# Performance work log

Measured on AMD Instinct MI355X. Metric: run time of the kernel, lower is better.

The kernel has to match this reference:

```python
import jax, jax.numpy as jnp
import numpy as np

B, T, V, E, H, L = 64, 512, 50000, 256, 256, 9


def _lstm_dir(x, w_ih, w_hh, b, reverse):
    # x: [B,T,I]; w_ih: [4H,I]; w_hh: [4H,H]; b: [4H]. PyTorch gate order i,f,g,o.
    Bm, Hm = x.shape[0], w_hh.shape[1]
    gx = jnp.einsum('bti,gi->btg', x, w_ih) + b  # [B,T,4H] precomputed input proj

    def step(carry, g_t):
        h, c = carry
        gates = g_t + h @ w_hh.T
        i, f, g, o = jnp.split(gates, 4, axis=-1)
        c = jax.nn.sigmoid(f) * c + jax.nn.sigmoid(i) * jnp.tanh(g)
        h = jax.nn.sigmoid(o) * jnp.tanh(c)
        return (h, c), h

    init = (jnp.zeros((Bm, Hm), x.dtype), jnp.zeros((Bm, Hm), x.dtype))
    _, hs = jax.lax.scan(step, init, jnp.swapaxes(gx, 0, 1), reverse=reverse)
    return jnp.swapaxes(hs, 0, 1)  # [B,T,H]


def _bilstm_layer(x, w_ih, w_hh, b):
    fwd = _lstm_dir(x, w_ih[0], w_hh[0], b[0], False)
    bwd = _lstm_dir(x, w_ih[1], w_hh[1], b[1], True)
    return jnp.concatenate([fwd, bwd], axis=-1)  # [B,T,2H]


def _crf_nll(emissions, labels, mask, trans, start_trans, end_trans):
    # emissions: [B,T,L]; labels: [B,T] int; mask: [B,T] (mask[:,0] assumed 1)
    maskf = mask.astype(emissions.dtype)
    # gold path score
    em_lab = jnp.take_along_axis(emissions, labels[..., None], axis=2)[..., 0]  # [B,T]
    trans_sc = trans[labels[:, :-1], labels[:, 1:]]  # [B,T-1]
    score = start_trans[labels[:, 0]] + em_lab[:, 0] \
        + jnp.sum((trans_sc + em_lab[:, 1:]) * maskf[:, 1:], axis=1)
    last_idx = jnp.sum(mask, axis=1).astype(jnp.int32) - 1
    last_lab = jnp.take_along_axis(labels, last_idx[:, None].astype(labels.dtype), axis=1)[:, 0]
    score = score + end_trans[last_lab]
    # log-partition via forward algorithm (scan over time)
    alpha0 = start_trans[None, :] + emissions[:, 0]  # [B,L]

    def step(alpha, xs):
        em_t, m_t = xs
        new = jax.nn.logsumexp(alpha[:, :, None] + trans[None], axis=1) + em_t
        alpha = jnp.where(m_t[:, None] > 0, new, alpha)
        return alpha, None

    alpha, _ = jax.lax.scan(
        step, alpha0,
        (jnp.swapaxes(emissions[:, 1:], 0, 1), jnp.swapaxes(mask[:, 1:], 0, 1)))
    logZ = jax.nn.logsumexp(alpha + end_trans[None, :], axis=1)  # [B]
    return -(score - logZ).mean()


def setup_inputs() -> dict:
    key = jax.random.key(0)
    ks = jax.random.split(key, 16)
    s = 0.05
    inp = {
        'input_ids': jax.random.randint(ks[0], (B, T), 0, V),
        'attention_mask': jnp.ones((B, T), jnp.int32),
        'labels': jax.random.randint(ks[1], (B, T), 0, L),
        'emb': jax.random.normal(ks[2], (V, E), jnp.float32) * s,
        # layer 0: input size E; layer 1: input size 2H. [dir, 4H, in]
        'w_ih0': jax.random.normal(ks[3], (2, 4 * H, E), jnp.float32) * s,
        'w_hh0': jax.random.normal(ks[4], (2, 4 * H, H), jnp.float32) * s,
        'b0': jax.random.normal(ks[5], (2, 4 * H), jnp.float32) * s,
        'w_ih1': jax.random.normal(ks[6], (2, 4 * H, 2 * H), jnp.float32) * s,
        'w_hh1': jax.random.normal(ks[7], (2, 4 * H, H), jnp.float32) * s,
        'b1': jax.random.normal(ks[8], (2, 4 * H), jnp.float32) * s,
        'lin_w': jax.random.normal(ks[9], (L, 2 * H), jnp.float32) * s,
        'lin_b': jax.random.normal(ks[10], (L,), jnp.float32) * s,
        'trans': jax.random.normal(ks[11], (L, L), jnp.float32) * 0.1,
        'start_trans': jax.random.normal(ks[12], (L,), jnp.float32) * 0.1,
        'end_trans': jax.random.normal(ks[13], (L,), jnp.float32) * 0.1,
    }
    return inp


def reference(input_ids, attention_mask, labels, emb, w_ih0, w_hh0, b0,
              w_ih1, w_hh1, b1, lin_w, lin_b, trans, start_trans, end_trans):
    x = emb[input_ids]                       # [B,T,E]
    x = _bilstm_layer(x, w_ih0, w_hh0, b0)   # [B,T,2H]
    x = _bilstm_layer(x, w_ih1, w_hh1, b1)   # [B,T,2H]
    emissions = x @ lin_w.T + lin_b          # [B,T,L]
    loss = _crf_nll(emissions, labels, attention_mask, trans, start_trans, end_trans)
    return loss
```

## Files before the change

### kernel.cpp

```cpp
#include <hip/hip_runtime.h>
#include <stdint.h>
#include <stddef.h>

#define B_ 64
#define T_ 512
#define E_ 256
#define H_ 256
#define L_ 9
#define BT (B_*T_)
#define G4 1024
#define N2 2048

typedef short    bf16x8  __attribute__((ext_vector_type(8)));
typedef float    f32x4   __attribute__((ext_vector_type(4)));
typedef int      i32x4   __attribute__((ext_vector_type(4)));
typedef int      i32x8   __attribute__((ext_vector_type(8)));
typedef unsigned short u16x8 __attribute__((ext_vector_type(8)));

__device__ __forceinline__ unsigned short f2bf(float x){
    unsigned u = __builtin_bit_cast(unsigned, x);
    u += 0x7fffu + ((u >> 16) & 1u);
    return (unsigned short)(u >> 16);
}
__device__ __forceinline__ float bf2f(unsigned short h){
    unsigned u = ((unsigned)h) << 16;
    return __builtin_bit_cast(float, u);
}

__device__ __forceinline__ unsigned char f32_e4m3(float x){
    unsigned b = __builtin_bit_cast(unsigned, x);
    unsigned s = b >> 31;
    float a = fabsf(x);
    if (a >= 448.f) return (unsigned char)((s<<7) | 0x7E);
    int E = (int)((b>>23)&255) - 127;
    if (E < -6) E = -6;
    int qi = (int)rintf(a * exp2f((float)(3 - E)));
    if (qi >= 16){ qi >>= 1; ++E; }
    if (qi == 0) return (unsigned char)(s<<7);
    unsigned mag = (qi >= 8) ? ((((unsigned)(E + 7)) << 3) | (unsigned)(qi - 8))
                             : (unsigned)qi;
    return (unsigned char)((s<<7) | mag);
}

__device__ __forceinline__ float sigm(float x){
    return __builtin_amdgcn_rcpf(1.f + __expf(-x));
}
__device__ __forceinline__ float tanh_(float x){
    float e = __expf(2.f*x);
    return 1.f - 2.f*__builtin_amdgcn_rcpf(e + 1.f);
}

__device__ __forceinline__ unsigned char f32_fp8(float x){
#if __has_builtin(__builtin_amdgcn_cvt_pk_fp8_f32)
    return (unsigned char)(__builtin_amdgcn_cvt_pk_fp8_f32(x, x, 0, false) & 0xff);
#else
    return f32_e4m3(x);
#endif
}

__device__ __forceinline__ void lds_load16(void* lds, const void* g){
    __builtin_amdgcn_global_load_lds(
        (const __attribute__((address_space(1))) void*)g,
        (__attribute__((address_space(3))) void*)lds, 16, 0, 0);
}

__device__ __forceinline__ void barrier_lds(){
    asm volatile("s_waitcnt lgkmcnt(0)" ::: "memory");
    __builtin_amdgcn_s_barrier();
    __builtin_amdgcn_sched_barrier(0);
}

__global__ void k_embed(const int* __restrict__ ids, const float* __restrict__ emb,
                        unsigned char* __restrict__ x0){
    int bt = blockIdx.x;
    int e  = threadIdx.x;
    int id = ids[bt];
    x0[(size_t)bt*E_ + e] = f32_e4m3(emb[(size_t)id*E_ + e]);
}

__global__ void k_pack_wih(const float* __restrict__ in, unsigned char* __restrict__ out, int K){
    int p = blockIdx.y;
    int k = blockIdx.x*256 + threadIdx.x;
    int dirc = p >> 10, pp = p & 1023;
    int wv = pp >> 7, rem = pp & 127;
    int ulx = rem >> 3, uh = (rem >> 2) & 1, g = rem & 3;
    int orig = dirc*1024 + g*256 + wv*32 + uh*16 + ulx;
    out[(size_t)p*K + k] = f32_e4m3(in[(size_t)orig*K + k]);
}

__global__ void k_pack_bias(const float* __restrict__ b, float* __restrict__ bp){
    int p = blockIdx.x*256 + threadIdx.x;
    int dirc = p >> 10, pp = p & 1023;
    int wv = pp >> 7, rem = pp & 127;
    int ulx = rem >> 3, uh = (rem >> 2) & 1, g = rem & 3;
    int orig = dirc*1024 + g*256 + wv*32 + uh*16 + ulx;
    bp[p] = b[orig];
}

__global__ void k_pack_wfp8(const float* __restrict__ whh, unsigned char* __restrict__ wpk){
    int idx = blockIdx.x*256 + threadIdx.x;
    int lane = idx & 63;
    int uh   = (idx >> 6) & 1;
    int g    = (idx >> 7) & 3;
    int kt   = (idx >> 9) & 1;
    int wv   = (idx >> 10) & 7;
    int dir  = (idx >> 13) & 1;
    int ulx = lane & 15, hi4 = lane >> 4;
    int row = g*256 + wv*32 + uh*16 + ulx;
    int k0 = kt*128 + hi4*32;
    const float* src = whh + ((size_t)dir*G4 + row)*H_ + k0;
    unsigned char* dst = wpk + (size_t)idx*32;
    #pragma unroll
    for (int q = 0; q < 32; ++q) dst[q] = f32_e4m3(src[q]);
}

__global__ __launch_bounds__(256) void k_gemm_fp8(const unsigned char* __restrict__ A,
                                                  const unsigned char* __restrict__ Bm,
                                                  const float* __restrict__ bias,
                                                  unsigned short* __restrict__ C,
                                                  int M, int N, int K){
    __shared__ __align__(16) unsigned char As[2][16384];
    __shared__ __align__(16) unsigned char Bs[2][16384];
    int tid = threadIdx.x, lane = tid & 63, w = tid >> 6;
    int wm = w >> 1, wn = w & 1;
    int nwg = gridDim.x, qch = nwg >> 3;
    int nid = (blockIdx.x & 7)*qch + (blockIdx.x >> 3);
    int tileM = (nid >> 4) * 128, tileN = (nid & 15) * 128;
    int nC = K >> 7;

    auto stage = [&](int c, int buf){
        #pragma unroll
        for (int p = 0; p < 4; ++p){
            int idx = (p*256 + tid)*16;
            int ks = idx >> 12, rem = idx & 4095, row = rem >> 5;
            int jsrc = (rem & 16) ^ ((row & 4) << 2);
            lds_load16(&As[buf][idx], A + (size_t)(tileM + row)*K + c*128 + ks*32 + jsrc);
            lds_load16(&Bs[buf][idx], Bm + (size_t)(tileN + row)*K + c*128 + ks*32 + jsrc);
        }
    };

    stage(0, 0);
    __syncthreads();
    f32x4 acc[4][4] = {};
    for (int c = 0; c < nC; ++c){
        int buf = c & 1;
        if (c + 1 < nC) stage(c + 1, buf ^ 1);
        int ks = lane >> 4, m15 = lane & 15;
        i32x8 af[4], bfv[4];
        #pragma unroll
        for (int mf = 0; mf < 4; ++mf){
            int r = wm*64 + mf*16 + m15;
            int base = ks*4096 + r*32, sw = (r & 4) << 2;
            i32x4 lo = *(const i32x4*)(&As[buf][base + sw]);
            i32x4 hi = *(const i32x4*)(&As[buf][base + (16 ^ sw)]);
            af[mf] = __builtin_shufflevector(lo, hi, 0,1,2,3,4,5,6,7);
        }
        #pragma unroll
        for (int nf = 0; nf < 4; ++nf){
            int r = wn*64 + nf*16 + m15;
            int base = ks*4096 + r*32, sw = (r & 4) << 2;
            i32x4 lo = *(const i32x4*)(&Bs[buf][base + sw]);
            i32x4 hi = *(const i32x4*)(&Bs[buf][base + (16 ^ sw)]);
            bfv[nf] = __builtin_shufflevector(lo, hi, 0,1,2,3,4,5,6,7);
        }
        #pragma unroll
        for (int mf = 0; mf < 4; ++mf)
            #pragma unroll
            for (int nf = 0; nf < 4; ++nf)
                acc[mf][nf] = __builtin_amdgcn_mfma_scale_f32_16x16x128_f8f6f4(
                                  af[mf], bfv[nf], acc[mf][nf],
                                  0, 0, 0, 0x7f7f7f7f, 0, 0x7f7f7f7f);
        __syncthreads();
    }
    #pragma unroll
    for (int mf = 0; mf < 4; ++mf){
        #pragma unroll
        for (int nf = 0; nf < 4; ++nf){
            int row0 = tileM + wm*64 + mf*16 + (lane >> 4)*4;
            int col  = tileN + wn*64 + nf*16 + (lane & 15);
            float bv = bias[col];
            #pragma unroll
            for (int r = 0; r < 4; ++r)
                C[(size_t)(row0 + r)*N + col] = f2bf(acc[mf][nf][r] + bv);
        }
    }
}

template<typename OutT>
__global__ __launch_bounds__(512, 2)
void k_rec_mfma(const unsigned short* __restrict__ gx,
                const unsigned char* __restrict__ wpk,
                OutT* __restrict__ out){
    int blk = blockIdx.x;
    int dir = blk & 1, bg = blk >> 1;
    int tid = threadIdx.x, lane = tid & 63, w = tid >> 6;
    int ul = lane & 15, hi4 = lane >> 4;
    int batch = bg*4 + hi4;

    __shared__ __align__(16) unsigned char hlds[2][32][16][8];
    {
        unsigned long long* hz = (unsigned long long*)hlds;
        for (int i = tid; i < 1024; i += 512) hz[i] = 0ull;
    }

    i32x8 wf[2][4][2];
    {
        const i32x8* wb = (const i32x8*)wpk;
        #pragma unroll
        for (int kt = 0; kt < 2; ++kt)
            #pragma unroll
            for (int g = 0; g < 4; ++g)
                #pragma unroll
                for (int uh = 0; uh < 2; ++uh)
                    wf[kt][g][uh] = wb[((((size_t)(dir*8 + w)*2 + kt)*4 + g)*2 + uh)*64 + lane];
    }
    __syncthreads();

    const unsigned short* gp = gx + (size_t)(batch*T_ + (dir ? T_-1 : 0))*N2
                                  + dir*1024 + w*128 + ul*8;
    ptrdiff_t dstep = dir ? -(ptrdiff_t)N2 : (ptrdiff_t)N2;

    u16x8 gxr = *(const u16x8*)gp;
    float c0 = 0.f, c1 = 0.f;
    int u0 = w*32 + ul, u1 = u0 + 16;
    OutT* ob = out + (size_t)batch*T_*512 + dir*256;

#define REC_STEP(SV, BUF)                                                          \
    {                                                                              \
        const unsigned long long* hrow = (const unsigned long long*)&hlds[BUF][0][0][0]; \
        unsigned long long a00 = hrow[(hi4*4 + 0)*16 + ul];                        \
        unsigned long long a01 = hrow[(hi4*4 + 1)*16 + ul];                        \
        unsigned long long a02 = hrow[(hi4*4 + 2)*16 + ul];                        \
        unsigned long long a03 = hrow[(hi4*4 + 3)*16 + ul];                        \
        unsigned long long a10 = hrow[(16 + hi4*4 + 0)*16 + ul];                   \
        unsigned long long a11 = hrow[(16 + hi4*4 + 1)*16 + ul];                   \
        unsigned long long a12 = hrow[(16 + hi4*4 + 2)*16 + ul];                   \
        unsigned long long a13 = hrow[(16 + hi4*4 + 3)*16 + ul];                   \
        i32x8 af0 = (i32x8){ (int)a00, (int)(a00>>32), (int)a01, (int)(a01>>32),   \
                             (int)a02, (int)(a02>>32), (int)a03, (int)(a03>>32) }; \
        i32x8 af1 = (i32x8){ (int)a10, (int)(a10>>32), (int)a11, (int)(a11>>32),   \
                             (int)a12, (int)(a12>>32), (int)a13, (int)(a13>>32) }; \
        gp += dstep;                                                               \
        u16x8 gxn = *(const u16x8*)gp;                                             \
        f32x4 acc0[4], acc1[4];                                                    \
        _Pragma("unroll")                                                          \
        for (int g = 0; g < 4; ++g){                                               \
            acc0[g] = (f32x4){ bf2f(gxr[g]),   0.f, 0.f, 0.f };                    \
            acc1[g] = (f32x4){ bf2f(gxr[4+g]), 0.f, 0.f, 0.f };                    \
        }                                                                          \
                                                          \
        __builtin_amdgcn_s_setprio(1);                                             \
        _Pragma("unroll")                                                          \
        for (int g = 0; g < 4; ++g)                                                \
            acc0[g] = __builtin_amdgcn_mfma_scale_f32_16x16x128_f8f6f4(            \
                          af0, wf[0][g][0], acc0[g], 0, 0, 0, 0x7f7f7f7f, 0, 0x7f7f7f7f); \
        _Pragma("unroll")                                                          \
        for (int g = 0; g < 4; ++g)                                                \
            acc0[g] = __builtin_amdgcn_mfma_scale_f32_16x16x128_f8f6f4(            \
                          af1, wf[1][g][0], acc0[g], 0, 0, 0, 0x7f7f7f7f, 0, 0x7f7f7f7f); \
        __builtin_amdgcn_s_setprio(0);                                             \
                                           \
        float h0;                                                                  \
        {                                                                          \
            float xi = acc0[0][0], xf = acc0[1][0], xg = acc0[2][0], xo = acc0[3][0]; \
            c0 = sigm(xf)*c0 + sigm(xi)*tanh_(xg);                                 \
            h0 = sigm(xo)*tanh_(c0);                                               \
        }                                                                          \
        unsigned char hb0 = f32_fp8(h0);                                           \
        hlds[BUF^1][u0>>3][hi4*4][u0&7] = hb0;                                     \
                                                          \
        __builtin_amdgcn_s_setprio(1);                                             \
        _Pragma("unroll")                                                          \
        for (int g = 0; g < 4; ++g)                                                \
            acc1[g] = __builtin_amdgcn_mfma_scale_f32_16x16x128_f8f6f4(            \
                          af0, wf[0][g][1], acc1[g], 0, 0, 0, 0x7f7f7f7f, 0, 0x7f7f7f7f); \
        _Pragma("unroll")                                                          \
        for (int g = 0; g < 4; ++g)                                                \
            acc1[g] = __builtin_amdgcn_mfma_scale_f32_16x16x128_f8f6f4(            \
                          af1, wf[1][g][1], acc1[g], 0, 0, 0, 0x7f7f7f7f, 0, 0x7f7f7f7f); \
        __builtin_amdgcn_s_setprio(0);                                             \
        float h1;                                                                  \
        {                                                                          \
            float xi = acc1[0][0], xf = acc1[1][0], xg = acc1[2][0], xo = acc1[3][0]; \
            c1 = sigm(xf)*c1 + sigm(xi)*tanh_(xg);                                 \
            h1 = sigm(xo)*tanh_(c1);                                               \
        }                                                                          \
        unsigned char hb1 = f32_fp8(h1);                                           \
        hlds[BUF^1][u1>>3][hi4*4][u1&7] = hb1;                                     \
        barrier_lds();                                                             \
                       \
        int tt = dir ? (T_-1-(SV)) : (SV);                                         \
        if constexpr (sizeof(OutT) == 1){                                          \
            ((unsigned char*)ob)[(size_t)tt*512 + u0] = hb0;                       \
            ((unsigned char*)ob)[(size_t)tt*512 + u1] = hb1;                       \
        } else {                                                                   \
            ob[(size_t)tt*512 + u0] = (OutT)f2bf(h0);                              \
            ob[(size_t)tt*512 + u1] = (OutT)f2bf(h1);                              \
        }                                                                          \
        gxr = gxn;                                                                 \
    }

    for (int s = 0; s < T_; s += 2){
        REC_STEP(s, 0)
        REC_STEP(s+1, 1)
    }
#undef REC_STEP
}

__global__ __launch_bounds__(256) void k_linear(const unsigned short* __restrict__ x,
                                                const float* __restrict__ w,
                                                const float* __restrict__ bias,
                                                float* __restrict__ em){
    int wv = threadIdx.x >> 6, lane = threadIdx.x & 63;
    int bt = blockIdx.x*4 + wv;
    u16x8 xv = *(const u16x8*)(x + (size_t)bt*(2*H_) + lane*8);
    float xf[8];
    #pragma unroll
    for (int j = 0; j < 8; ++j) xf[j] = bf2f(xv[j]);
    #pragma unroll
    for (int l = 0; l < L_; ++l){
        const float4* wp = (const float4*)(w + (size_t)l*(2*H_) + lane*8);
        float4 wa = wp[0], wb = wp[1];
        float p = xf[0]*wa.x + xf[1]*wa.y + xf[2]*wa.z + xf[3]*wa.w
                + xf[4]*wb.x + xf[5]*wb.y + xf[6]*wb.z + xf[7]*wb.w;
        #pragma unroll
        for (int o = 32; o; o >>= 1) p += __shfl_xor(p, o);
        if (lane == 0) em[(size_t)bt*L_ + l] = p + bias[l];
    }
}

__global__ void k_crf(const float* __restrict__ em, const int* __restrict__ labels,
                      const int* __restrict__ mask, const float* __restrict__ trans,
                      const float* __restrict__ st, const float* __restrict__ et,
                      float* __restrict__ out){
    int b = blockIdx.x, lane = threadIdx.x;
    __shared__ float tr[L_*L_];
    for (int i = lane; i < L_*L_; i += 64) tr[i] = trans[i];
    __syncthreads();
    const float* e  = em + (size_t)b*T_*L_;
    const int* lab  = labels + b*T_;
    const int* mk   = mask + b*T_;
    float sc = 0.f; int msum = 0;
    for (int t = lane; t < T_; t += 64){
        msum += mk[t];
        if (t >= 1)
            sc += (tr[lab[t-1]*L_ + lab[t]] + e[t*L_ + lab[t]]) * (float)mk[t];
    }
    #pragma unroll
    for (int o = 32; o; o >>= 1){ sc += __shfl_xor(sc, o); msum += __shfl_xor(msum, o); }
    int lj = lane < L_ ? lane : 0;
    float alpha = (lane < L_) ? (st[lj] + e[lj]) : -3.0e38f;
    for (int t = 1; t < T_; ++t){
        float v[L_]; float m = -3.0e38f;
        #pragma unroll
        for (int i = 0; i < L_; ++i){
            float ai = __shfl(alpha, i);
            v[i] = ai + tr[i*L_ + lj];
            m = fmaxf(m, v[i]);
        }
        float ssum = 0.f;
        #pragma unroll
        for (int i = 0; i < L_; ++i) ssum += __expf(v[i] - m);
        float nw = m + __logf(ssum) + e[t*L_ + lj];
        if (lane < L_ && mk[t] > 0) alpha = nw;
    }
    float av = (lane < L_) ? alpha + et[lj] : -3.0e38f;
    float m2 = av;
    #pragma unroll
    for (int o = 32; o; o >>= 1) m2 = fmaxf(m2, __shfl_xor(m2, o));
    float s2 = (lane < L_) ? __expf(av - m2) : 0.f;
    #pragma unroll
    for (int o = 32; o; o >>= 1) s2 += __shfl_xor(s2, o);
    if (lane == 0){
        float logZ = m2 + __logf(s2);
        int last = msum - 1;
        float score = sc + st[lab[0]] + e[lab[0]] + et[lab[last]];
        atomicAdd(out, (logZ - score) * (1.f/(float)B_));
    }
}

extern "C" void kernel_launch(void* const* d_in, const int* in_sizes, int n_in,
                              void* d_out, int out_size, void* d_ws, size_t ws_size,
                              hipStream_t stream){
    (void)in_sizes; (void)n_in; (void)out_size; (void)ws_size;
    const int*   ids    = (const int*)d_in[0];
    const int*   amask  = (const int*)d_in[1];
    const int*   labels = (const int*)d_in[2];
    const float* emb    = (const float*)d_in[3];
    const float* w_ih0  = (const float*)d_in[4];
    const float* w_hh0  = (const float*)d_in[5];
    const float* b0     = (const float*)d_in[6];
    const float* w_ih1  = (const float*)d_in[7];
    const float* w_hh1  = (const float*)d_in[8];
    const float* b1     = (const float*)d_in[9];
    const float* lin_w  = (const float*)d_in[10];
    const float* lin_b  = (const float*)d_in[11];
    const float* trans  = (const float*)d_in[12];
    const float* st     = (const float*)d_in[13];
    const float* et     = (const float*)d_in[14];
    float* out = (float*)d_out;

    char* ws = (char*)d_ws;
    size_t o = 0;
    auto alloc = [&](size_t bytes)->char*{
        char* p = ws + o; o = (o + bytes + 255) & ~(size_t)255; return p;
    };
    unsigned char*  x0    = (unsigned char*)alloc((size_t)BT*E_);
    unsigned char*  wih0p = (unsigned char*)alloc((size_t)N2*E_);
    unsigned char*  wih1p = (unsigned char*)alloc((size_t)N2*512);
    unsigned char*  wpk0  = (unsigned char*)alloc(16384*32);
    unsigned char*  wpk1  = (unsigned char*)alloc(16384*32);
    float*          bp0   = (float*)alloc(N2*4);
    float*          bp1   = (float*)alloc(N2*4);
    unsigned short* gx    = (unsigned short*)alloc((size_t)BT*N2*2);
    unsigned char*  xc1   = (unsigned char*)alloc((size_t)BT*512);
    unsigned short* xc2   = (unsigned short*)alloc((size_t)BT*512*2);
    float*          em    = (float*)alloc((size_t)BT*L_*4 + 1024);

    hipMemsetAsync(d_out, 0, sizeof(float), stream);

    k_pack_wih<<<dim3(E_/256, N2), 256, 0, stream>>>(w_ih0, wih0p, E_);
    k_pack_wih<<<dim3(512/256, N2), 256, 0, stream>>>(w_ih1, wih1p, 512);
    k_pack_bias<<<N2/256, 256, 0, stream>>>(b0, bp0);
    k_pack_bias<<<N2/256, 256, 0, stream>>>(b1, bp1);
    k_pack_wfp8<<<16384/256, 256, 0, stream>>>(w_hh0, wpk0);
    k_pack_wfp8<<<16384/256, 256, 0, stream>>>(w_hh1, wpk1);
    k_embed<<<BT, E_, 0, stream>>>(ids, emb, x0);

    k_gemm_fp8<<<4096, 256, 0, stream>>>(x0, wih0p, bp0, gx, BT, N2, E_);
    k_rec_mfma<unsigned char><<<32, 512, 0, stream>>>(gx, wpk0, xc1);
    k_gemm_fp8<<<4096, 256, 0, stream>>>(xc1, wih1p, bp1, gx, BT, N2, 512);
    k_rec_mfma<unsigned short><<<32, 512, 0, stream>>>(gx, wpk1, xc2);

    k_linear<<<BT/4, 256, 0, stream>>>(xc2, lin_w, lin_b, em);
    k_crf<<<B_, 64, 0, stream>>>(em, labels, amask, trans, st, et, out);
}
```

Measured before the change: 1.408 ms.

## Reorder hidden-state LDS layout, interleave MFMA chains, and move barrier after stores

Changes the shared-memory layout of the fp8 hidden state so each lane reads its A-fragment with a contiguous, conflict-free pattern. The two independent MFMA accumulator chains are now interleaved to hide MFMA latency, and the setprio hints are removed. The barrier moves after the global output stores so those stores overlap the wait. The layout remap must keep the K-ordering consistent with the prepacked weight fragments, and dropping the priority hints may change how the waves are scheduled.

```diff
diff --git a/kernel.cpp b/kernel.cpp
--- a/kernel.cpp
+++ b/kernel.cpp
@@ -197,7 +197,7 @@
     int ul = lane & 15, hi4 = lane >> 4;
     int batch = bg*4 + hi4;
 
-    __shared__ __align__(16) unsigned char hlds[2][32][16][8];
+    __shared__ __align__(16) unsigned char hlds[2][2][4][4][16][8];
     {
         unsigned long long* hz = (unsigned long long*)hlds;
         for (int i = tid; i < 1024; i += 512) hz[i] = 0ull;
@@ -223,19 +223,20 @@
     u16x8 gxr = *(const u16x8*)gp;
     float c0 = 0.f, c1 = 0.f;
     int u0 = w*32 + ul, u1 = u0 + 16;
+    int wkt = w >> 2, wkg = w & 3, wj0 = ul >> 3, wj1 = 2 + (ul >> 3), wbyt = ul & 7, wrow = hi4*4;
     OutT* ob = out + (size_t)batch*T_*512 + dir*256;
 
 #define REC_STEP(SV, BUF)                                                          \
     {                                                                              \
-        const unsigned long long* hrow = (const unsigned long long*)&hlds[BUF][0][0][0]; \
-        unsigned long long a00 = hrow[(hi4*4 + 0)*16 + ul];                        \
-        unsigned long long a01 = hrow[(hi4*4 + 1)*16 + ul];                        \
-        unsigned long long a02 = hrow[(hi4*4 + 2)*16 + ul];                        \
-        unsigned long long a03 = hrow[(hi4*4 + 3)*16 + ul];                        \
-        unsigned long long a10 = hrow[(16 + hi4*4 + 0)*16 + ul];                   \
-        unsigned long long a11 = hrow[(16 + hi4*4 + 1)*16 + ul];                   \
-        unsigned long long a12 = hrow[(16 + hi4*4 + 2)*16 + ul];                   \
-        unsigned long long a13 = hrow[(16 + hi4*4 + 3)*16 + ul];                   \
+        const unsigned long long* hb = (const unsigned long long*)&hlds[BUF][0][0][0][0][0]; \
+        unsigned long long a00 = hb[  0 + hi4*16 + ul];                            \
+        unsigned long long a01 = hb[ 64 + hi4*16 + ul];                            \
+        unsigned long long a02 = hb[128 + hi4*16 + ul];                            \
+        unsigned long long a03 = hb[192 + hi4*16 + ul];                            \
+        unsigned long long a10 = hb[256 + hi4*16 + ul];                            \
+        unsigned long long a11 = hb[320 + hi4*16 + ul];                            \
+        unsigned long long a12 = hb[384 + hi4*16 + ul];                            \
+        unsigned long long a13 = hb[448 + hi4*16 + ul];                            \
         i32x8 af0 = (i32x8){ (int)a00, (int)(a00>>32), (int)a01, (int)(a01>>32),   \
                              (int)a02, (int)(a02>>32), (int)a03, (int)(a03>>32) }; \
         i32x8 af1 = (i32x8){ (int)a10, (int)(a10>>32), (int)a11, (int)(a11>>32),   \
@@ -248,47 +249,35 @@
             acc0[g] = (f32x4){ bf2f(gxr[g]),   0.f, 0.f, 0.f };                    \
             acc1[g] = (f32x4){ bf2f(gxr[4+g]), 0.f, 0.f, 0.f };                    \
         }                                                                          \
-                                                          \
-        __builtin_amdgcn_s_setprio(1);                                             \
         _Pragma("unroll")                                                          \
-        for (int g = 0; g < 4; ++g)                                                \
+        for (int g = 0; g < 4; ++g){                                               \
             acc0[g] = __builtin_amdgcn_mfma_scale_f32_16x16x128_f8f6f4(            \
                           af0, wf[0][g][0], acc0[g], 0, 0, 0, 0x7f7f7f7f, 0, 0x7f7f7f7f); \
+            acc1[g] = __builtin_amdgcn_mfma_scale_f32_16x16x128_f8f6f4(            \
+                          af0, wf[0][g][1], acc1[g], 0, 0, 0, 0x7f7f7f7f, 0, 0x7f7f7f7f); \
+        }                                                                          \
         _Pragma("unroll")                                                          \
-        for (int g = 0; g < 4; ++g)                                                \
+        for (int g = 0; g < 4; ++g){                                               \
             acc0[g] = __builtin_amdgcn_mfma_scale_f32_16x16x128_f8f6f4(            \
                           af1, wf[1][g][0], acc0[g], 0, 0, 0, 0x7f7f7f7f, 0, 0x7f7f7f7f); \
-        __builtin_amdgcn_s_setprio(0);                                             \
-                                           \
-        float h0;                                                                  \
+            acc1[g] = __builtin_amdgcn_mfma_scale_f32_16x16x128_f8f6f4(            \
+                          af1, wf[1][g][1], acc1[g], 0, 0, 0, 0x7f7f7f7f, 0, 0x7f7f7f7f); \
+        }                                                                          \
+        float h0, h1;                                                              \
         {                                                                          \
             float xi = acc0[0][0], xf = acc0[1][0], xg = acc0[2][0], xo = acc0[3][0]; \
             c0 = sigm(xf)*c0 + sigm(xi)*tanh_(xg);                                 \
             h0 = sigm(xo)*tanh_(c0);                                               \
         }                                                                          \
-        unsigned char hb0 = f32_fp8(h0);                                           \
-        hlds[BUF^1][u0>>3][hi4*4][u0&7] = hb0;                                     \
-                                                          \
-        __builtin_amdgcn_s_setprio(1);                                             \
-        _Pragma("unroll")                                                          \
-        for (int g = 0; g < 4; ++g)                                                \
-            acc1[g] = __builtin_amdgcn_mfma_scale_f32_16x16x128_f8f6f4(            \
-                          af0, wf[0][g][1], acc1[g], 0, 0, 0, 0x7f7f7f7f, 0, 0x7f7f7f7f); \
-        _Pragma("unroll")                                                          \
-        for (int g = 0; g < 4; ++g)                                                \
-            acc1[g] = __builtin_amdgcn_mfma_scale_f32_16x16x128_f8f6f4(            \
-                          af1, wf[1][g][1], acc1[g], 0, 0, 0, 0x7f7f7f7f, 0, 0x7f7f7f7f); \
-        __builtin_amdgcn_s_setprio(0);                                             \
-        float h1;                                                                  \
         {                                                                          \
             float xi = acc1[0][0], xf = acc1[1][0], xg = acc1[2][0], xo = acc1[3][0]; \
             c1 = sigm(xf)*c1 + sigm(xi)*tanh_(xg);                                 \
             h1 = sigm(xo)*tanh_(c1);                                               \
         }                                                                          \
+        unsigned char hb0 = f32_fp8(h0);                                           \
         unsigned char hb1 = f32_fp8(h1);                                           \
-        hlds[BUF^1][u1>>3][hi4*4][u1&7] = hb1;                                     \
-        barrier_lds();                                                             \
-                       \
+        hlds[BUF^1][wkt][wj0][wkg][wrow][wbyt] = hb0;                              \
+        hlds[BUF^1][wkt][wj1][wkg][wrow][wbyt] = hb1;                              \
         int tt = dir ? (T_-1-(SV)) : (SV);                                         \
         if constexpr (sizeof(OutT) == 1){                                          \
             ((unsigned char*)ob)[(size_t)tt*512 + u0] = hb0;                       \
@@ -298,6 +287,7 @@
             ob[(size_t)tt*512 + u1] = (OutT)f2bf(h1);                              \
         }                                                                          \
         gxr = gxn;                                                                 \
+        barrier_lds();                                                             \
     }
 
     for (int s = 0; s < T_; s += 2){
```

New measurement: 1.427 ms. About the same (+1.4%).
